# Performance work log

Measured on AMD Instinct MI355X. Metric: run time of the kernel, lower is better.

Reference implementation:

```python
import jax, jax.numpy as jnp
import numpy as np

N = 100000
E = 1600000
G = 100
HEADS = 4
CH = 32
POS = 16
IN_DIM = 128
OUT_DIM = 64
NEG_SLOPE = 0.2
BN_EPS = 1e-5


def _grid_positions(batch):
    # replicate _get_normalized_positions: per-graph ceil(sqrt(count)) grid, vectorized
    counts = jax.ops.segment_sum(jnp.ones(N, jnp.int32), batch, num_segments=G)
    starts = jnp.concatenate([jnp.zeros(1, jnp.int32), jnp.cumsum(counts)[:-1].astype(jnp.int32)])
    local = jnp.arange(N, dtype=jnp.int32) - starts[batch]
    cnt = counts[batch]
    gs = jnp.ceil(jnp.sqrt(cnt.astype(jnp.float32))).astype(jnp.int32)
    row = local // gs
    col = local % gs
    denom = jnp.maximum(gs - 1, 1).astype(jnp.float32)
    return jnp.stack([row.astype(jnp.float32) / denom, col.astype(jnp.float32) / denom], axis=1)


def _seg_softmax(alpha, dst):
    # numerically-stable softmax over edges grouped by destination node
    amax = jax.ops.segment_max(alpha, dst, num_segments=N)
    amax = jnp.where(jnp.isfinite(amax), amax, 0.0)
    e = jnp.exp(alpha - amax[dst])
    s = jax.ops.segment_sum(e, dst, num_segments=N)
    return e / (s[dst] + 1e-16)


def _gat_layer(h, pos, src, dst, W, att, Wp, b):
    xt = (h @ W.T).reshape(N, HEADS, CH)                       # [N,H,C]
    pe = (pos[dst] - pos[src]) @ Wp.T                          # [E',P]
    a = att[0]                                                 # [H, 2C+P]
    # decompose (cat(x_src, x_dst, pe) * att).sum(-1) to avoid [E',H,2C+P] intermediate
    a_src = jnp.einsum('nhc,hc->nh', xt, a[:, :CH])
    a_dst = jnp.einsum('nhc,hc->nh', xt, a[:, CH:2 * CH])
    alpha = a_src[src] + a_dst[dst] + pe @ a[:, 2 * CH:].T     # [E',H]
    alpha = jnp.where(alpha > 0, alpha, NEG_SLOPE * alpha)     # leaky_relu
    alpha = _seg_softmax(alpha, dst)
    # faithful to source: message uses x[dst_idx], aggregated onto dst
    out = jax.ops.segment_sum(xt[dst] * alpha[:, :, None], dst, num_segments=N)
    return out.reshape(N, HEADS * CH) + b


def _batchnorm(h, g, b):
    mu = h.mean(0)
    var = h.var(0)  # biased, matches torch BN training-mode normalization
    return (h - mu) / jnp.sqrt(var + BN_EPS) * g + b


def setup_inputs() -> dict:
    key = jax.random.key(0)
    ks = jax.random.split(key, 20)
    s = 0.1
    return {
        'x': jax.random.normal(ks[0], (N, IN_DIM), jnp.float32),
        'edge_index': jax.random.randint(ks[1], (2, E), 0, N, jnp.int32),
        'batch': (jnp.arange(N, dtype=jnp.int32) // (N // G)).astype(jnp.int32),
        'pe_W': jax.random.normal(ks[2], (POS, 2), jnp.float32) * s,
        'pe_b': jax.random.normal(ks[3], (POS,), jnp.float32) * s,
        'lin_W0': jax.random.normal(ks[4], (HEADS * CH, IN_DIM + POS), jnp.float32) * s,
        'att0': jax.random.normal(ks[5], (1, HEADS, 2 * CH + POS), jnp.float32) * s,
        'posW0': jax.random.normal(ks[6], (POS, 2), jnp.float32) * s,
        'bias0': jax.random.normal(ks[7], (HEADS * CH,), jnp.float32) * s,
        'bn_g0': jax.random.uniform(ks[8], (HEADS * CH,), jnp.float32, 0.5, 1.5),
        'bn_b0': jax.random.normal(ks[9], (HEADS * CH,), jnp.float32) * s,
        'lin_W1': jax.random.normal(ks[10], (HEADS * CH, HEADS * CH), jnp.float32) * s,
        'att1': jax.random.normal(ks[11], (1, HEADS, 2 * CH + POS), jnp.float32) * s,
        'posW1': jax.random.normal(ks[12], (POS, 2), jnp.float32) * s,
        'bias1': jax.random.normal(ks[13], (HEADS * CH,), jnp.float32) * s,
        'bn_g1': jax.random.uniform(ks[14], (HEADS * CH,), jnp.float32, 0.5, 1.5),
        'bn_b1': jax.random.normal(ks[15], (HEADS * CH,), jnp.float32) * s,
        'fc_W': jax.random.normal(ks[16], (OUT_DIM, HEADS * CH), jnp.float32) * s,
        'fc_b': jax.random.normal(ks[17], (OUT_DIM,), jnp.float32) * s,
    }


def reference(x, edge_index, batch, pe_W, pe_b,
              lin_W0, att0, posW0, bias0, bn_g0, bn_b0,
              lin_W1, att1, posW1, bias1, bn_g1, bn_b1,
              fc_W, fc_b):
    pos = _grid_positions(batch)
    h = jnp.concatenate([x, pos @ pe_W.T + pe_b], axis=1)      # PositionalEncoding
    loop = jnp.arange(N, dtype=edge_index.dtype)
    src = jnp.concatenate([edge_index[0], loop])               # add_self_loops
    dst = jnp.concatenate([edge_index[1], loop])
    layers = ((lin_W0, att0, posW0, bias0, bn_g0, bn_b0),
              (lin_W1, att1, posW1, bias1, bn_g1, bn_b1))
    for (W, att, Wp, b, g, bb) in layers:
        h = _gat_layer(h, pos, src, dst, W, att, Wp, b)
        h = _batchnorm(h, g, bb)
        h = jax.nn.elu(h)
        # dropout: eval mode (identity); _refine_positions is identity
    counts = jax.ops.segment_sum(jnp.ones(N, jnp.float32), batch, num_segments=G)
    pooled = jax.ops.segment_sum(h, batch, num_segments=G) / counts[:, None]
    return pooled @ fc_W.T + fc_b
```

## Files before the change

kernel.cpp:

```cpp
#include <hip/hip_runtime.h>

#define NN 100000

typedef __bf16 bf16x8 __attribute__((ext_vector_type(8)));
typedef float  f32x4  __attribute__((ext_vector_type(4)));

__device__ __forceinline__ float b2f(ushort u) {
    union { unsigned int i; float f; } v; v.i = ((unsigned int)u) << 16; return v.f;
}
__device__ __forceinline__ ushort f2b(float f) {
    union { float f; unsigned int i; } v; v.f = f;
    unsigned int r = (v.i + 0x7fffu + ((v.i >> 16) & 1u)) >> 16;
    return (ushort)r;
}
__device__ __forceinline__ float elu_f(float v) {
    return v > 0.0f ? v : __expf(v) - 1.0f;
}

__global__ __launch_bounds__(256)
void zero_k(const float* __restrict__ W0, const float* __restrict__ W1,
            float* __restrict__ stats, float* __restrict__ out,
            ushort* __restrict__ wb0, ushort* __restrict__ wb1) {
    int i = blockIdx.x * 256 + threadIdx.x;
    if (i < 14592) { if (i < 8192) stats[i] = 0.0f; else out[i - 8192] = 0.0f; }
    if (i < 18432) wb0[i] = f2b(W0[i]);
    else if (i < 34816) wb1[i - 18432] = f2b(W1[i - 18432]);
}

__device__ __forceinline__ void build_af(bf16x8 af[2][5], const float* __restrict__ x,
                                         const float* __restrict__ peW,
                                         const float* __restrict__ peB,
                                         int blockM, int wm, int m, int kq) {
    #pragma unroll
    for (int mi = 0; mi < 2; ++mi) {
        const int gr = blockM + wm + mi * 16 + m;
        const bool ok = gr < NN;
        #pragma unroll
        for (int kc = 0; kc < 4; ++kc) {
            const int k0 = kc * 32 + kq * 8;
            float4 v0 = make_float4(0.f, 0.f, 0.f, 0.f), v1 = v0;
            if (ok) {
                v0 = *(const float4*)(x + (size_t)gr * 128 + k0);
                v1 = *(const float4*)(x + (size_t)gr * 128 + k0 + 4);
            }
            ushort u[8] = { f2b(v0.x), f2b(v0.y), f2b(v0.z), f2b(v0.w),
                            f2b(v1.x), f2b(v1.y), f2b(v1.z), f2b(v1.w) };
            af[mi][kc] = *(bf16x8*)u;
        }
        {
            ushort u[8] = {0, 0, 0, 0, 0, 0, 0, 0};
            if (kq < 2 && ok) {
                const int local = gr - (gr / 1000) * 1000;
                const float px = (float)(local >> 5) * (1.0f / 31.0f);
                const float py = (float)(local & 31) * (1.0f / 31.0f);
                #pragma unroll
                for (int j = 0; j < 8; ++j) {
                    int p = kq * 8 + j;
                    u[j] = f2b(px * peW[2 * p] + py * peW[2 * p + 1] + peB[p]);
                }
            }
            af[mi][4] = *(bf16x8*)u;
        }
    }
}

__device__ __forceinline__ void mfma_s1(f32x4 acc[2][4], bf16x8 af[2][5],
                                        const ushort* __restrict__ wb0,
                                        int wn, int m, int kq) {
    #pragma unroll
    for (int kc = 0; kc < 5; ++kc) {
        const int k0 = kc * 32 + kq * 8;
        bf16x8 bf[4];
        #pragma unroll
        for (int ni = 0; ni < 4; ++ni) {
            if (k0 < 144)
                bf[ni] = *(const bf16x8*)(wb0 + (wn + ni * 16 + m) * 144 + k0);
            else {
                ushort z[8] = {0, 0, 0, 0, 0, 0, 0, 0};
                bf[ni] = *(bf16x8*)z;
            }
        }
        #pragma unroll
        for (int mi = 0; mi < 2; ++mi)
            #pragma unroll
            for (int ni = 0; ni < 4; ++ni)
                acc[mi][ni] = __builtin_amdgcn_mfma_f32_16x16x32_bf16(
                    af[mi][kc], bf[ni], acc[mi][ni], 0, 0, 0);
    }
}

__device__ __forceinline__ void stats_epi(const f32x4 acc[2][4], float* smS, float* smQ,
                                          float* __restrict__ statsOut,
                                          int t, int wave, int lane, int wn, int m,
                                          int bid) {
    float s[4] = {0, 0, 0, 0}, q[4] = {0, 0, 0, 0};
    #pragma unroll
    for (int mi = 0; mi < 2; ++mi)
        #pragma unroll
        for (int ni = 0; ni < 4; ++ni)
            #pragma unroll
            for (int r = 0; r < 4; ++r) {
                const float z = acc[mi][ni][r];
                s[ni] += z; q[ni] += z * z;
            }
    #pragma unroll
    for (int ni = 0; ni < 4; ++ni) {
        s[ni] += __shfl_xor(s[ni], 16); s[ni] += __shfl_xor(s[ni], 32);
        q[ni] += __shfl_xor(q[ni], 16); q[ni] += __shfl_xor(q[ni], 32);
    }
    if (lane < 16) {
        #pragma unroll
        for (int ni = 0; ni < 4; ++ni) {
            const int idx = wave * 64 + ni * 16 + m;
            smS[idx] = s[ni]; smQ[idx] = q[ni];
        }
    }
    __syncthreads();
    if (t < 128) {
        const int base = (t >> 6) * 128 + (t & 63);
        float S = smS[base] + smS[base + 64];
        float Q = smQ[base] + smQ[base + 64];
        float* sl = statsOut + (bid & 15) * 256;
        atomicAdd(sl + t, S);
        atomicAdd(sl + 128 + t, Q);
    }
}

__global__ __launch_bounds__(256)
void gemm1s_k(const float* __restrict__ x, const ushort* __restrict__ wb0,
              const float* __restrict__ peW, const float* __restrict__ peB,
              float* __restrict__ stats1)
{
    __shared__ float smS[256], smQ[256];
    const int t = threadIdx.x;
    const int blockM = blockIdx.x * 64;
    const int wave = t >> 6, lane = t & 63;
    const int wm = (wave & 1) * 32, wn = (wave >> 1) * 64;
    const int m = lane & 15, kq = lane >> 4;

    bf16x8 af[2][5];
    build_af(af, x, peW, peB, blockM, wm, m, kq);
    f32x4 acc[2][4];
    #pragma unroll
    for (int mi = 0; mi < 2; ++mi)
        #pragma unroll
        for (int ni = 0; ni < 4; ++ni) acc[mi][ni] = (f32x4){0.f, 0.f, 0.f, 0.f};
    mfma_s1(acc, af, wb0, wn, m, kq);
    stats_epi(acc, smS, smQ, stats1, t, wave, lane, wn, m, blockIdx.x);
}

__global__ __launch_bounds__(256, 2)
void gemm2f_k(const float* __restrict__ x, const ushort* __restrict__ wb0,
              const ushort* __restrict__ wb1,
              const float* __restrict__ peW, const float* __restrict__ peB,
              const float* __restrict__ stats1, const float* __restrict__ g0,
              const float* __restrict__ bb0, ushort* __restrict__ Z,
              float* __restrict__ stats2)
{
    __shared__ ushort h1S[64 * 136];
    __shared__ float smS[256], smQ[256];
    __shared__ float smSS[256];
    const int t = threadIdx.x;
    const int blockM = blockIdx.x * 64;
    const int wave = t >> 6, lane = t & 63;
    const int wm = (wave & 1) * 32, wn = (wave >> 1) * 64;
    const int m = lane & 15, kq = lane >> 4;

    if (t < 128) {
        float S = 0.f, Q = 0.f;
        #pragma unroll
        for (int k = 0; k < 16; ++k) { S += stats1[k * 256 + t]; Q += stats1[k * 256 + 128 + t]; }
        float mu = S * (1.0f / NN);
        float var = fmaxf(Q * (1.0f / NN) - mu * mu, 0.0f);
        float istd = rsqrtf(var + 1e-5f);
        float sc = g0[t] * istd;
        smSS[t] = sc; smSS[128 + t] = bb0[t] - mu * sc;
    }

    bf16x8 af[2][5];
    build_af(af, x, peW, peB, blockM, wm, m, kq);
    f32x4 acc1[2][4];
    #pragma unroll
    for (int mi = 0; mi < 2; ++mi)
        #pragma unroll
        for (int ni = 0; ni < 4; ++ni) acc1[mi][ni] = (f32x4){0.f, 0.f, 0.f, 0.f};
    mfma_s1(acc1, af, wb0, wn, m, kq);

    __syncthreads();

    #pragma unroll
    for (int mi = 0; mi < 2; ++mi)
        #pragma unroll
        for (int ni = 0; ni < 4; ++ni) {
            const int col = wn + ni * 16 + m;
            const float sc = smSS[col], sh = smSS[128 + col];
            const int rb = wm + mi * 16 + kq * 4;
            #pragma unroll
            for (int r = 0; r < 4; ++r) {
                const bool ok = (blockM + rb + r) < NN;
                const float h = elu_f(acc1[mi][ni][r] * sc + sh);
                h1S[(rb + r) * 136 + col] = ok ? f2b(h) : (ushort)0;
            }
        }
    __syncthreads();

    f32x4 acc2[2][4];
    #pragma unroll
    for (int mi = 0; mi < 2; ++mi)
        #pragma unroll
        for (int ni = 0; ni < 4; ++ni) acc2[mi][ni] = (f32x4){0.f, 0.f, 0.f, 0.f};
    #pragma unroll
    for (int kc = 0; kc < 4; ++kc) {
        const int k0 = kc * 32 + kq * 8;
        bf16x8 a2[2], bf[4];
        #pragma unroll
        for (int mi = 0; mi < 2; ++mi)
            a2[mi] = *(const bf16x8*)(h1S + (wm + mi * 16 + m) * 136 + k0);
        #pragma unroll
        for (int ni = 0; ni < 4; ++ni)
            bf[ni] = *(const bf16x8*)(wb1 + (wn + ni * 16 + m) * 128 + k0);
        #pragma unroll
        for (int mi = 0; mi < 2; ++mi)
            #pragma unroll
            for (int ni = 0; ni < 4; ++ni)
                acc2[mi][ni] = __builtin_amdgcn_mfma_f32_16x16x32_bf16(
                    a2[mi], bf[ni], acc2[mi][ni], 0, 0, 0);
    }

    stats_epi(acc2, smS, smQ, stats2, t, wave, lane, wn, m, blockIdx.x);

    ushort* ZS = h1S;
    #pragma unroll
    for (int mi = 0; mi < 2; ++mi)
        #pragma unroll
        for (int ni = 0; ni < 4; ++ni) {
            const int col = wn + ni * 16 + m;
            const int rb = wm + mi * 16 + kq * 4;
            #pragma unroll
            for (int r = 0; r < 4; ++r)
                ZS[(rb + r) * 136 + col] = f2b(acc2[mi][ni][r]);
        }
    __syncthreads();
    #pragma unroll
    for (int i = 0; i < 4; ++i) {
        const int idx = i * 256 + t;
        const int row = idx >> 4, c16 = idx & 15;
        const int gr = blockM + row;
        if (gr < NN)
            *(uint4*)(Z + (size_t)gr * 128 + c16 * 8) =
                *(const uint4*)(ZS + row * 136 + c16 * 8);
    }
}

__global__ __launch_bounds__(256)
void poolfc_k(const ushort* __restrict__ Z, const float* __restrict__ stats,
              const float* __restrict__ g, const float* __restrict__ bb,
              const float* __restrict__ fcW, const float* __restrict__ fcB,
              float* __restrict__ out) {
    __shared__ float smSS[256];
    __shared__ float smT[16 * 128];
    __shared__ float smP[128];
    const int t = threadIdx.x;
    if (t < 128) {
        float S = 0.f, Q = 0.f;
        #pragma unroll
        for (int k = 0; k < 16; ++k) { S += stats[k * 256 + t]; Q += stats[k * 256 + 128 + t]; }
        float mu = S * (1.0f / NN);
        float var = fmaxf(Q * (1.0f / NN) - mu * mu, 0.0f);
        float istd = rsqrtf(var + 1e-5f);
        float sc = g[t] * istd;
        smSS[t] = sc; smSS[128 + t] = bb[t] - mu * sc;
    }
    __syncthreads();
    const int gg = blockIdx.x >> 2, part = blockIdx.x & 3;
    const int r16 = t >> 4, c8 = t & 15;
    const int r0 = gg * 1000 + part * 250;
    float sc[8], sh[8];
    #pragma unroll
    for (int j = 0; j < 8; ++j) { sc[j] = smSS[c8 * 8 + j]; sh[j] = smSS[128 + c8 * 8 + j]; }
    float a[8] = {0, 0, 0, 0, 0, 0, 0, 0};
    #pragma unroll
    for (int i = 0; i < 16; ++i) {
        if (i < 15 || r16 < 10) {
            const uint4 v = *(const uint4*)(Z + ((size_t)(r0 + i * 16 + r16)) * 128 + c8 * 8);
            const ushort* u = (const ushort*)&v;
            #pragma unroll
            for (int j = 0; j < 8; ++j) a[j] += elu_f(b2f(u[j]) * sc[j] + sh[j]);
        }
    }
    #pragma unroll
    for (int j = 0; j < 8; ++j) smT[r16 * 128 + c8 * 8 + j] = a[j];
    __syncthreads();
    if (t < 128) {
        float S = 0.0f;
        #pragma unroll
        for (int k = 0; k < 16; ++k) S += smT[k * 128 + t];
        smP[t] = S;
    }
    __syncthreads();
    if (t < 64) {
        float d = 0.0f;
        #pragma unroll
        for (int j4 = 0; j4 < 32; ++j4) {
            float4 w = *(const float4*)(fcW + t * 128 + j4 * 4);
            d += smP[j4 * 4 + 0] * w.x + smP[j4 * 4 + 1] * w.y
               + smP[j4 * 4 + 2] * w.z + smP[j4 * 4 + 3] * w.w;
        }
        float acc = d * (1.0f / 1000.0f) + (part == 0 ? fcB[t] : 0.0f);
        atomicAdd(&out[gg * 64 + t], acc);
    }
}

extern "C" void kernel_launch(void* const* d_in, const int* in_sizes, int n_in,
                              void* d_out, int out_size, void* d_ws, size_t ws_size,
                              hipStream_t stream) {
    const float* x   = (const float*)d_in[0];
    const float* peW = (const float*)d_in[3];
    const float* peB = (const float*)d_in[4];
    const float* W0  = (const float*)d_in[5];
    const float* g0  = (const float*)d_in[9];
    const float* bb0 = (const float*)d_in[10];
    const float* W1  = (const float*)d_in[11];
    const float* g1  = (const float*)d_in[15];
    const float* bb1 = (const float*)d_in[16];
    const float* fcW = (const float*)d_in[17];
    const float* fcB = (const float*)d_in[18];
    float* out = (float*)d_out;

    float* wsF = (float*)d_ws;
    float* stats1 = wsF;
    float* stats2 = wsF + 4096;
    ushort* wb0 = (ushort*)((char*)d_ws + 65536);
    ushort* wb1 = (ushort*)((char*)d_ws + 131072);
    ushort* z2 = (ushort*)((char*)d_ws + 262144);

    zero_k<<<136, 256, 0, stream>>>(W0, W1, stats1, out, wb0, wb1);
    gemm1s_k<<<1563, 256, 0, stream>>>(x, wb0, peW, peB, stats1);
    gemm2f_k<<<1563, 256, 0, stream>>>(x, wb0, wb1, peW, peB,
                                       stats1, g0, bb0, z2, stats2);
    poolfc_k<<<400, 256, 0, stream>>>(z2, stats2, g1, bb1, fcW, fcB, out);
}
```

Measured before the change: 190.9 us.

## Fuse two GEMM passes into a persistent kernel with a grid-wide barrier

Replaces the separate stats-only GEMM kernel and the second fused GEMM kernel with one persistent kernel of 512 blocks. Each block first runs the layer-1 GEMM over its 3–4 tiles to gather BN statistics, waits at an atomic-counter grid barrier, then recomputes those tiles and runs the layer-2 path. This drops one kernel launch and its tail. The cost is a spin barrier that assumes all 512 blocks are resident at once and gives up after a bounded number of polls, so results could be wrong if co-residency fails.

```diff
diff --git a/kernel.cpp b/kernel.cpp
--- a/kernel.cpp
+++ b/kernel.cpp
@@ -19,10 +19,11 @@
 
 __global__ __launch_bounds__(256)
 void zero_k(const float* __restrict__ W0, const float* __restrict__ W1,
-            float* __restrict__ stats, float* __restrict__ out,
+            float* __restrict__ wsF, float* __restrict__ out,
             ushort* __restrict__ wb0, ushort* __restrict__ wb1) {
     int i = blockIdx.x * 256 + threadIdx.x;
-    if (i < 14592) { if (i < 8192) stats[i] = 0.0f; else out[i - 8192] = 0.0f; }
+    if (i < 8448) wsF[i] = 0.0f;
+    else if (i < 14848) out[i - 8448] = 0.0f;
     if (i < 18432) wb0[i] = f2b(W0[i]);
     else if (i < 34816) wb1[i - 18432] = f2b(W1[i - 18432]);
 }
@@ -92,7 +93,7 @@
 __device__ __forceinline__ void stats_epi(const f32x4 acc[2][4], float* smS, float* smQ,
                                           float* __restrict__ statsOut,
                                           int t, int wave, int lane, int wn, int m,
-                                          int bid) {
+                                          int slab) {
     float s[4] = {0, 0, 0, 0}, q[4] = {0, 0, 0, 0};
     #pragma unroll
     for (int mi = 0; mi < 2; ++mi)
@@ -120,51 +121,57 @@
         const int base = (t >> 6) * 128 + (t & 63);
         float S = smS[base] + smS[base + 64];
         float Q = smQ[base] + smQ[base + 64];
-        float* sl = statsOut + (bid & 15) * 256;
+        float* sl = statsOut + (slab & 15) * 256;
         atomicAdd(sl + t, S);
         atomicAdd(sl + 128 + t, Q);
     }
 }
 
-__global__ __launch_bounds__(256)
-void gemm1s_k(const float* __restrict__ x, const ushort* __restrict__ wb0,
-              const float* __restrict__ peW, const float* __restrict__ peB,
-              float* __restrict__ stats1)
-{
-    __shared__ float smS[256], smQ[256];
-    const int t = threadIdx.x;
-    const int blockM = blockIdx.x * 64;
-    const int wave = t >> 6, lane = t & 63;
-    const int wm = (wave & 1) * 32, wn = (wave >> 1) * 64;
-    const int m = lane & 15, kq = lane >> 4;
-
-    bf16x8 af[2][5];
-    build_af(af, x, peW, peB, blockM, wm, m, kq);
-    f32x4 acc[2][4];
-    #pragma unroll
-    for (int mi = 0; mi < 2; ++mi)
-        #pragma unroll
-        for (int ni = 0; ni < 4; ++ni) acc[mi][ni] = (f32x4){0.f, 0.f, 0.f, 0.f};
-    mfma_s1(acc, af, wb0, wn, m, kq);
-    stats_epi(acc, smS, smQ, stats1, t, wave, lane, wn, m, blockIdx.x);
-}
-
 __global__ __launch_bounds__(256, 2)
-void gemm2f_k(const float* __restrict__ x, const ushort* __restrict__ wb0,
-              const ushort* __restrict__ wb1,
-              const float* __restrict__ peW, const float* __restrict__ peB,
-              const float* __restrict__ stats1, const float* __restrict__ g0,
-              const float* __restrict__ bb0, ushort* __restrict__ Z,
-              float* __restrict__ stats2)
+void fused_k(const float* __restrict__ x, const ushort* __restrict__ wb0,
+             const ushort* __restrict__ wb1,
+             const float* __restrict__ peW, const float* __restrict__ peB,
+             const float* __restrict__ g0, const float* __restrict__ bb0,
+             ushort* __restrict__ Z, float* __restrict__ stats1,
+             float* __restrict__ stats2, int* __restrict__ cnt)
 {
     __shared__ ushort h1S[64 * 136];
     __shared__ float smS[256], smQ[256];
     __shared__ float smSS[256];
     const int t = threadIdx.x;
-    const int blockM = blockIdx.x * 64;
+    const int bid = blockIdx.x;
     const int wave = t >> 6, lane = t & 63;
     const int wm = (wave & 1) * 32, wn = (wave >> 1) * 64;
     const int m = lane & 15, kq = lane >> 4;
+    const int nTiles = (bid < 27) ? 4 : 3;
+
+    for (int it = 0; it < nTiles; ++it) {
+        const int tile = (it < 3) ? bid * 3 + it : 1536 + bid;
+        const int blockM = tile * 64;
+        bf16x8 af[2][5];
+        build_af(af, x, peW, peB, blockM, wm, m, kq);
+        f32x4 acc[2][4];
+        #pragma unroll
+        for (int mi = 0; mi < 2; ++mi)
+            #pragma unroll
+            for (int ni = 0; ni < 4; ++ni) acc[mi][ni] = (f32x4){0.f, 0.f, 0.f, 0.f};
+        mfma_s1(acc, af, wb0, wn, m, kq);
+        stats_epi(acc, smS, smQ, stats1, t, wave, lane, wn, m, tile);
+        __syncthreads();
+    }
+
+    __syncthreads();
+    if (t == 0) {
+        __threadfence();
+        atomicAdd(cnt, 1);
+        int polls = 0;
+        while (atomicAdd(cnt, 0) < 512 && polls < 200000) {
+            ++polls;
+            __builtin_amdgcn_s_sleep(8);
+        }
+        __threadfence();
+    }
+    __syncthreads();
 
     if (t < 128) {
         float S = 0.f, Q = 0.f;
@@ -176,79 +183,83 @@
         float sc = g0[t] * istd;
         smSS[t] = sc; smSS[128 + t] = bb0[t] - mu * sc;
     }
-
-    bf16x8 af[2][5];
-    build_af(af, x, peW, peB, blockM, wm, m, kq);
-    f32x4 acc1[2][4];
-    #pragma unroll
-    for (int mi = 0; mi < 2; ++mi)
-        #pragma unroll
-        for (int ni = 0; ni < 4; ++ni) acc1[mi][ni] = (f32x4){0.f, 0.f, 0.f, 0.f};
-    mfma_s1(acc1, af, wb0, wn, m, kq);
-
-    __syncthreads();
-
-    #pragma unroll
-    for (int mi = 0; mi < 2; ++mi)
-        #pragma unroll
-        for (int ni = 0; ni < 4; ++ni) {
-            const int col = wn + ni * 16 + m;
-            const float sc = smSS[col], sh = smSS[128 + col];
-            const int rb = wm + mi * 16 + kq * 4;
-            #pragma unroll
-            for (int r = 0; r < 4; ++r) {
-                const bool ok = (blockM + rb + r) < NN;
-                const float h = elu_f(acc1[mi][ni][r] * sc + sh);
-                h1S[(rb + r) * 136 + col] = ok ? f2b(h) : (ushort)0;
-            }
-        }
-    __syncthreads();
-
-    f32x4 acc2[2][4];
-    #pragma unroll
-    for (int mi = 0; mi < 2; ++mi)
-        #pragma unroll
-        for (int ni = 0; ni < 4; ++ni) acc2[mi][ni] = (f32x4){0.f, 0.f, 0.f, 0.f};
-    #pragma unroll
-    for (int kc = 0; kc < 4; ++kc) {
-        const int k0 = kc * 32 + kq * 8;
-        bf16x8 a2[2], bf[4];
-        #pragma unroll
-        for (int mi = 0; mi < 2; ++mi)
-            a2[mi] = *(const bf16x8*)(h1S + (wm + mi * 16 + m) * 136 + k0);
-        #pragma unroll
-        for (int ni = 0; ni < 4; ++ni)
-            bf[ni] = *(const bf16x8*)(wb1 + (wn + ni * 16 + m) * 128 + k0);
-        #pragma unroll
-        for (int mi = 0; mi < 2; ++mi)
+    __syncthreads();
+
+    for (int it = 0; it < nTiles; ++it) {
+        const int tile = (it < 3) ? bid * 3 + it : 1536 + bid;
+        const int blockM = tile * 64;
+        bf16x8 af[2][5];
+        build_af(af, x, peW, peB, blockM, wm, m, kq);
+        f32x4 acc1[2][4];
+        #pragma unroll
+        for (int mi = 0; mi < 2; ++mi)
+            #pragma unroll
+            for (int ni = 0; ni < 4; ++ni) acc1[mi][ni] = (f32x4){0.f, 0.f, 0.f, 0.f};
+        mfma_s1(acc1, af, wb0, wn, m, kq);
+
+        #pragma unroll
+        for (int mi = 0; mi < 2; ++mi)
+            #pragma unroll
+            for (int ni = 0; ni < 4; ++ni) {
+                const int col = wn + ni * 16 + m;
+                const float sc = smSS[col], sh = smSS[128 + col];
+                const int rb = wm + mi * 16 + kq * 4;
+                #pragma unroll
+                for (int r = 0; r < 4; ++r) {
+                    const bool ok = (blockM + rb + r) < NN;
+                    const float h = elu_f(acc1[mi][ni][r] * sc + sh);
+                    h1S[(rb + r) * 136 + col] = ok ? f2b(h) : (ushort)0;
+                }
+            }
+        __syncthreads();
+
+        f32x4 acc2[2][4];
+        #pragma unroll
+        for (int mi = 0; mi < 2; ++mi)
+            #pragma unroll
+            for (int ni = 0; ni < 4; ++ni) acc2[mi][ni] = (f32x4){0.f, 0.f, 0.f, 0.f};
+        #pragma unroll
+        for (int kc = 0; kc < 4; ++kc) {
+            const int k0 = kc * 32 + kq * 8;
+            bf16x8 a2[2], bf[4];
+            #pragma unroll
+            for (int mi = 0; mi < 2; ++mi)
+                a2[mi] = *(const bf16x8*)(h1S + (wm + mi * 16 + m) * 136 + k0);
             #pragma unroll
             for (int ni = 0; ni < 4; ++ni)
-                acc2[mi][ni] = __builtin_amdgcn_mfma_f32_16x16x32_bf16(
-                    a2[mi], bf[ni], acc2[mi][ni], 0, 0, 0);
-    }
-
-    stats_epi(acc2, smS, smQ, stats2, t, wave, lane, wn, m, blockIdx.x);
-
-    ushort* ZS = h1S;
-    #pragma unroll
-    for (int mi = 0; mi < 2; ++mi)
-        #pragma unroll
-        for (int ni = 0; ni < 4; ++ni) {
-            const int col = wn + ni * 16 + m;
-            const int rb = wm + mi * 16 + kq * 4;
-            #pragma unroll
-            for (int r = 0; r < 4; ++r)
-                ZS[(rb + r) * 136 + col] = f2b(acc2[mi][ni][r]);
-        }
-    __syncthreads();
-    #pragma unroll
-    for (int i = 0; i < 4; ++i) {
-        const int idx = i * 256 + t;
-        const int row = idx >> 4, c16 = idx & 15;
-        const int gr = blockM + row;
-        if (gr < NN)
-            *(uint4*)(Z + (size_t)gr * 128 + c16 * 8) =
-                *(const uint4*)(ZS + row * 136 + c16 * 8);
+                bf[ni] = *(const bf16x8*)(wb1 + (wn + ni * 16 + m) * 128 + k0);
+            #pragma unroll
+            for (int mi = 0; mi < 2; ++mi)
+                #pragma unroll
+                for (int ni = 0; ni < 4; ++ni)
+                    acc2[mi][ni] = __builtin_amdgcn_mfma_f32_16x16x32_bf16(
+                        a2[mi], bf[ni], acc2[mi][ni], 0, 0, 0);
+        }
+
+        stats_epi(acc2, smS, smQ, stats2, t, wave, lane, wn, m, tile);
+
+        ushort* ZS = h1S;
+        #pragma unroll
+        for (int mi = 0; mi < 2; ++mi)
+            #pragma unroll
+            for (int ni = 0; ni < 4; ++ni) {
+                const int col = wn + ni * 16 + m;
+                const int rb = wm + mi * 16 + kq * 4;
+                #pragma unroll
+                for (int r = 0; r < 4; ++r)
+                    ZS[(rb + r) * 136 + col] = f2b(acc2[mi][ni][r]);
+            }
+        __syncthreads();
+        #pragma unroll
+        for (int i = 0; i < 4; ++i) {
+            const int idx = i * 256 + t;
+            const int row = idx >> 4, c16 = idx & 15;
+            const int gr = blockM + row;
+            if (gr < NN)
+                *(uint4*)(Z + (size_t)gr * 128 + c16 * 8) =
+                    *(const uint4*)(ZS + row * 136 + c16 * 8);
+        }
+        __syncthreads();
     }
 }
 
@@ -330,13 +341,13 @@
     float* wsF = (float*)d_ws;
     float* stats1 = wsF;
     float* stats2 = wsF + 4096;
+    int*   cnt    = (int*)(wsF + 8192);
     ushort* wb0 = (ushort*)((char*)d_ws + 65536);
     ushort* wb1 = (ushort*)((char*)d_ws + 131072);
     ushort* z2 = (ushort*)((char*)d_ws + 262144);
 
-    zero_k<<<136, 256, 0, stream>>>(W0, W1, stats1, out, wb0, wb1);
-    gemm1s_k<<<1563, 256, 0, stream>>>(x, wb0, peW, peB, stats1);
-    gemm2f_k<<<1563, 256, 0, stream>>>(x, wb0, wb1, peW, peB,
-                                       stats1, g0, bb0, z2, stats2);
+    zero_k<<<136, 256, 0, stream>>>(W0, W1, wsF, out, wb0, wb1);
+    fused_k<<<512, 256, 0, stream>>>(x, wb0, wb1, peW, peB, g0, bb0,
+                                     z2, stats1, stats2, cnt);
     poolfc_k<<<400, 256, 0, stream>>>(z2, stats2, g1, bb1, fcW, fcB, out);
 }
```

Result: slower. 256.1 us (+34.2%).
